# Optimization experiments

Hardware: AMD Instinct MI355X
Metric: run time of the kernel (lower is better)

The kernel has to match this reference:

```python
import jax, jax.numpy as jnp
import numpy as np


def setup_inputs() -> dict:
    key = jax.random.key(0)
    k1, k2, k3, k4 = jax.random.split(key, 4)
    N_NODES, N_RELS, N_TRIPLES, H = 100000, 100000, 300000, 256
    node_states = jax.random.normal(k1, (N_NODES, H), dtype=jnp.float32)
    rel_states = jax.random.normal(k2, (N_RELS, H), dtype=jnp.float32)
    triples = jax.random.randint(k3, (N_TRIPLES, 3), 0, N_NODES, dtype=jnp.int64)
    # nn.Linear(2H, H): weight (H, 2H) in torch; store transposed (2H, H) for x @ W
    W = jax.random.normal(k4, (2 * H, H), dtype=jnp.float32) * (1.0 / np.sqrt(2 * H))
    b = jnp.zeros((H,), dtype=jnp.float32)
    return {"node_states": node_states, "rel_states": rel_states, "triples": triples, "W": W, "b": b}


def reference(node_states, rel_states, triples, W, b):
    # triples columns: (subj_idx, rel_idx, obj_idx)
    subj_idx, rel_idx, obj_idx = triples[:, 0], triples[:, 1], triples[:, 2]
    rel = rel_states[rel_idx]                              # (T, H)
    msg_s2o = node_states[subj_idx] + rel                  # (T, H)
    msg_o2s = node_states[obj_idx] + rel                   # (T, H)
    agg = jnp.zeros_like(node_states)
    agg = agg.at[obj_idx].add(msg_s2o)
    agg = agg.at[subj_idx].add(msg_o2s)
    h = jnp.concatenate([node_states, agg], axis=-1)       # (N, 2H)
    h = h @ W + b                                          # (N, H)
    h = jax.nn.silu(h)
    return node_states + h
```

## Files before the change

kernel.cpp:

```cpp
#include <hip/hip_runtime.h>

#define H 256
typedef unsigned int  uint;
typedef unsigned short ushort;
typedef float  floatx4 __attribute__((ext_vector_type(4)));
typedef short  shortx8 __attribute__((ext_vector_type(8)));

__device__ __forceinline__ ushort bf16rn(float f) {
    uint u = __float_as_uint(f);
    u += 0x7FFF + ((u >> 16) & 1);
    return (ushort)(u >> 16);
}
__device__ __forceinline__ uint pkbf2(float a, float b) {
    return (uint)bf16rn(a) | ((uint)bf16rn(b) << 16);
}
__device__ __forceinline__ void atomic_pk_bf16(void* addr, uint v) {
    asm volatile("global_atomic_pk_add_bf16 %0, %1, off" :: "v"(addr), "v"(v) : "memory");
}
__device__ __forceinline__ void glds16(const void* g, void* l) {
    __builtin_amdgcn_global_load_lds(
        (__attribute__((address_space(1))) void*)(unsigned long long)(g),
        (__attribute__((address_space(3))) void*)(l), 16, 0, 0);
}

__global__ __launch_bounds__(256) void wt_kernel(const float* __restrict__ W,
                                                 ushort* __restrict__ Wt) {
    int k = blockIdx.x;
    int n = threadIdx.x;
    Wt[(size_t)n * 512 + k] = bf16rn(W[(size_t)k * H + n]);
}

__global__ __launch_bounds__(256) void scatter_kernel(
    const float* __restrict__ ns, const float* __restrict__ rs,
    const int* __restrict__ trip, char* __restrict__ outbase, int n_trip)
{
    int t = blockIdx.x * 2 + (threadIdx.x >> 7);
    if (t >= n_trip) return;
    int p = threadIdx.x & 127;
    int s = trip[3 * t + 0];
    int r = trip[3 * t + 1];
    int o = trip[3 * t + 2];
    float2 vs = ((const float2*)ns)[(size_t)s * 128 + p];
    float2 vo = ((const float2*)ns)[(size_t)o * 128 + p];
    float2 vr = ((const float2*)rs)[(size_t)r * 128 + p];
    uint m_s2o = pkbf2(vs.x + vr.x, vs.y + vr.y);
    uint m_o2s = pkbf2(vo.x + vr.x, vo.y + vr.y);
    atomic_pk_bf16(outbase + (size_t)o * 1024 + p * 4, m_s2o);
    atomic_pk_bf16(outbase + (size_t)s * 1024 + p * 4, m_o2s);
}

__global__ __launch_bounds__(256) void gemm_kernel(
    const float* __restrict__ ns, const float* __restrict__ aggf,
    const ushort* __restrict__ Wt, const float* __restrict__ bias,
    float* __restrict__ out, int M)
{
    __shared__ __align__(16) ushort AsP[64 * 40];
    __shared__ __align__(16) ushort AsU[64 * 32];
    __shared__ __align__(16) ushort Bs [256 * 32];

    const int tid  = threadIdx.x;
    const int wave = tid >> 6;
    const int lane = tid & 63;
    const int fm = lane & 15, fq = lane >> 4;
    const int rowBase = blockIdx.x * 64;

    floatx4 acc[4][4] = {};

    const int am = tid >> 2, akq = tid & 3;
    int arow = rowBase + am; if (arow >= M) arow = M - 1;
    const float* aptrA = ns + (size_t)arow * H + akq * 8;
    const char*  aggp  = (const char*)aggf + (size_t)arow * 1024 + akq * 16;
    const char*  wtp   = (const char*)Wt;

#pragma unroll
    for (int kt = 0; kt < 8; ++kt) {
        __syncthreads();
        float4 v0 = *(const float4*)(aptrA + kt * 32);
        float4 v1 = *(const float4*)(aptrA + kt * 32 + 4);
#pragma unroll
        for (int j = 0; j < 4; ++j)
            glds16(wtp + (size_t)(j * 64 + am) * 1024 + kt * 64 + akq * 16,
                   &Bs[j * 2048 + tid * 8]);
        uint4 pk;
        pk.x = pkbf2(v0.x, v0.y); pk.y = pkbf2(v0.z, v0.w);
        pk.z = pkbf2(v1.x, v1.y); pk.w = pkbf2(v1.z, v1.w);
        *(uint4*)&AsP[am * 40 + akq * 8] = pk;
        __syncthreads();

        shortx8 aF[4], bF[4];
#pragma unroll
        for (int mi = 0; mi < 4; ++mi)
            aF[mi] = *(const shortx8*)&AsP[(mi * 16 + fm) * 40 + fq * 8];
#pragma unroll
        for (int ni = 0; ni < 4; ++ni)
            bF[ni] = *(const shortx8*)&Bs[(wave * 64 + ni * 16 + fm) * 32 + fq * 8];
#pragma unroll
        for (int mi = 0; mi < 4; ++mi)
#pragma unroll
            for (int ni = 0; ni < 4; ++ni)
                acc[mi][ni] = __builtin_amdgcn_mfma_f32_16x16x32_bf16(
                    aF[mi], bF[ni], acc[mi][ni], 0, 0, 0);
    }

#pragma unroll
    for (int kt = 0; kt < 8; ++kt) {
        __syncthreads();
        glds16(aggp + kt * 64, &AsU[tid * 8]);
#pragma unroll
        for (int j = 0; j < 4; ++j)
            glds16(wtp + (size_t)(j * 64 + am) * 1024 + (kt + 8) * 64 + akq * 16,
                   &Bs[j * 2048 + tid * 8]);
        __syncthreads();

        shortx8 aF[4], bF[4];
#pragma unroll
        for (int mi = 0; mi < 4; ++mi)
            aF[mi] = *(const shortx8*)&AsU[(mi * 16 + fm) * 32 + fq * 8];
#pragma unroll
        for (int ni = 0; ni < 4; ++ni)
            bF[ni] = *(const shortx8*)&Bs[(wave * 64 + ni * 16 + fm) * 32 + fq * 8];
#pragma unroll
        for (int mi = 0; mi < 4; ++mi)
#pragma unroll
            for (int ni = 0; ni < 4; ++ni)
                acc[mi][ni] = __builtin_amdgcn_mfma_f32_16x16x32_bf16(
                    aF[mi], bF[ni], acc[mi][ni], 0, 0, 0);
    }

#pragma unroll
    for (int mi = 0; mi < 4; ++mi) {
#pragma unroll
        for (int ni = 0; ni < 4; ++ni) {
            int col = wave * 64 + ni * 16 + fm;
            float bc = bias[col];
#pragma unroll
            for (int r = 0; r < 4; ++r) {
                int row = rowBase + mi * 16 + fq * 4 + r;
                if (row < M) {
                    float x = acc[mi][ni][r] + bc;
                    float sg = 1.f / (1.f + __expf(-x));
                    out[(size_t)row * H + col] = ns[(size_t)row * H + col] + x * sg;
                }
            }
        }
    }
}

extern "C" void kernel_launch(void* const* d_in, const int* in_sizes, int n_in,
                              void* d_out, int out_size, void* d_ws, size_t ws_size,
                              hipStream_t stream)
{
    const float* ns   = (const float*)d_in[0];
    const float* rs   = (const float*)d_in[1];
    const int*   tp   = (const int*)d_in[2];
    const float* Wm   = (const float*)d_in[3];
    const float* bias = (const float*)d_in[4];
    const int M      = in_sizes[0] / H;
    const int n_trip = in_sizes[2] / 3;
    float*  out = (float*)d_out;
    ushort* Wt  = (ushort*)d_ws;

    hipMemsetAsync(d_out, 0, (size_t)M * H * sizeof(float), stream);
    wt_kernel<<<dim3(512), dim3(256), 0, stream>>>(Wm, Wt);
    scatter_kernel<<<dim3((n_trip + 1) / 2), dim3(256), 0, stream>>>(
        ns, rs, tp, (char*)d_out, n_trip);
    gemm_kernel<<<dim3((M + 63) / 64), dim3(256), 0, stream>>>(
        ns, out, Wt, bias, out, M);
}
```

Before: 549.0 us.

## Precast node states to bf16 in output buffer and drop LDS staging in GEMM

A prep kernel replaces the memset. It zeroes the aggregation half of each output row and writes a bf16 copy of the node states into the unused upper half. The GEMM then loads its A and B MFMA fragments straight from global memory. This removes the LDS tiles, the per-k-step barriers, and the fp32-to-bf16 packing inside the GEMM. In exchange there is an extra pass over node states before the scatter, and the GEMM now relies on L2 for fragment reuse instead of shared memory.

```diff
diff --git a/kernel.cpp b/kernel.cpp
--- a/kernel.cpp
+++ b/kernel.cpp
@@ -17,10 +17,17 @@
 __device__ __forceinline__ void atomic_pk_bf16(void* addr, uint v) {
     asm volatile("global_atomic_pk_add_bf16 %0, %1, off" :: "v"(addr), "v"(v) : "memory");
 }
-__device__ __forceinline__ void glds16(const void* g, void* l) {
-    __builtin_amdgcn_global_load_lds(
-        (__attribute__((address_space(1))) void*)(unsigned long long)(g),
-        (__attribute__((address_space(3))) void*)(l), 16, 0, 0);
+
+__global__ __launch_bounds__(256) void prep_kernel(
+    const float* __restrict__ ns, char* __restrict__ outb, int M)
+{
+    long j = (long)blockIdx.x * 256 + threadIdx.x;
+    long row = j >> 7;
+    int  p   = (int)(j & 127);
+    if (row >= M) return;
+    float2 v = ((const float2*)ns)[row * 128 + p];
+    *(uint*)(outb + row * 1024 + p * 4)       = 0u;
+    *(uint*)(outb + row * 1024 + 512 + p * 4) = pkbf2(v.x, v.y);
 }
 
 __global__ __launch_bounds__(256) void wt_kernel(const float* __restrict__ W,
@@ -50,50 +57,58 @@
 }
 
 __global__ __launch_bounds__(256) void gemm_kernel(
-    const float* __restrict__ ns, const float* __restrict__ aggf,
+    const float* __restrict__ ns, const char* __restrict__ rowbuf,
     const ushort* __restrict__ Wt, const float* __restrict__ bias,
     float* __restrict__ out, int M)
 {
-    __shared__ __align__(16) ushort AsP[64 * 40];
-    __shared__ __align__(16) ushort AsU[64 * 32];
-    __shared__ __align__(16) ushort Bs [256 * 32];
-
     const int tid  = threadIdx.x;
     const int wave = tid >> 6;
     const int lane = tid & 63;
     const int fm = lane & 15, fq = lane >> 4;
     const int rowBase = blockIdx.x * 64;
 
+    long aoff[4];
+#pragma unroll
+    for (int mi = 0; mi < 4; ++mi) {
+        int r = rowBase + mi * 16 + fm;
+        if (r >= M) r = M - 1;
+        aoff[mi] = (long)r * 1024;
+    }
+    const char* wb = (const char*)Wt;
+    const long  bn[4] = { (long)(wave * 64 +  0 + fm) * 1024,
+                          (long)(wave * 64 + 16 + fm) * 1024,
+                          (long)(wave * 64 + 32 + fm) * 1024,
+                          (long)(wave * 64 + 48 + fm) * 1024 };
+
     floatx4 acc[4][4] = {};
-
-    const int am = tid >> 2, akq = tid & 3;
-    int arow = rowBase + am; if (arow >= M) arow = M - 1;
-    const float* aptrA = ns + (size_t)arow * H + akq * 8;
-    const char*  aggp  = (const char*)aggf + (size_t)arow * 1024 + akq * 16;
-    const char*  wtp   = (const char*)Wt;
 
 #pragma unroll
     for (int kt = 0; kt < 8; ++kt) {
-        __syncthreads();
-        float4 v0 = *(const float4*)(aptrA + kt * 32);
-        float4 v1 = *(const float4*)(aptrA + kt * 32 + 4);
-#pragma unroll
-        for (int j = 0; j < 4; ++j)
-            glds16(wtp + (size_t)(j * 64 + am) * 1024 + kt * 64 + akq * 16,
-                   &Bs[j * 2048 + tid * 8]);
-        uint4 pk;
-        pk.x = pkbf2(v0.x, v0.y); pk.y = pkbf2(v0.z, v0.w);
-        pk.z = pkbf2(v1.x, v1.y); pk.w = pkbf2(v1.z, v1.w);
-        *(uint4*)&AsP[am * 40 + akq * 8] = pk;
-        __syncthreads();
-
+        const int ko = kt * 64 + fq * 16;
         shortx8 aF[4], bF[4];
 #pragma unroll
         for (int mi = 0; mi < 4; ++mi)
-            aF[mi] = *(const shortx8*)&AsP[(mi * 16 + fm) * 40 + fq * 8];
+            aF[mi] = *(const shortx8*)(rowbuf + aoff[mi] + 512 + ko);
 #pragma unroll
         for (int ni = 0; ni < 4; ++ni)
-            bF[ni] = *(const shortx8*)&Bs[(wave * 64 + ni * 16 + fm) * 32 + fq * 8];
+            bF[ni] = *(const shortx8*)(wb + bn[ni] + ko);
+#pragma unroll
+        for (int mi = 0; mi < 4; ++mi)
+#pragma unroll
+            for (int ni = 0; ni < 4; ++ni)
+                acc[mi][ni] = __builtin_amdgcn_mfma_f32_16x16x32_bf16(
+                    aF[mi], bF[ni], acc[mi][ni], 0, 0, 0);
+    }
+#pragma unroll
+    for (int kt = 0; kt < 8; ++kt) {
+        const int ko = kt * 64 + fq * 16;
+        shortx8 aF[4], bF[4];
+#pragma unroll
+        for (int mi = 0; mi < 4; ++mi)
+            aF[mi] = *(const shortx8*)(rowbuf + aoff[mi] + ko);
+#pragma unroll
+        for (int ni = 0; ni < 4; ++ni)
+            bF[ni] = *(const shortx8*)(wb + bn[ni] + 512 + ko);
 #pragma unroll
         for (int mi = 0; mi < 4; ++mi)
 #pragma unroll
@@ -102,30 +117,7 @@
                     aF[mi], bF[ni], acc[mi][ni], 0, 0, 0);
     }
 
-#pragma unroll
-    for (int kt = 0; kt < 8; ++kt) {
-        __syncthreads();
-        glds16(aggp + kt * 64, &AsU[tid * 8]);
-#pragma unroll
-        for (int j = 0; j < 4; ++j)
-            glds16(wtp + (size_t)(j * 64 + am) * 1024 + (kt + 8) * 64 + akq * 16,
-                   &Bs[j * 2048 + tid * 8]);
-        __syncthreads();
-
-        shortx8 aF[4], bF[4];
-#pragma unroll
-        for (int mi = 0; mi < 4; ++mi)
-            aF[mi] = *(const shortx8*)&AsU[(mi * 16 + fm) * 32 + fq * 8];
-#pragma unroll
-        for (int ni = 0; ni < 4; ++ni)
-            bF[ni] = *(const shortx8*)&Bs[(wave * 64 + ni * 16 + fm) * 32 + fq * 8];
-#pragma unroll
-        for (int mi = 0; mi < 4; ++mi)
-#pragma unroll
-            for (int ni = 0; ni < 4; ++ni)
-                acc[mi][ni] = __builtin_amdgcn_mfma_f32_16x16x32_bf16(
-                    aF[mi], bF[ni], acc[mi][ni], 0, 0, 0);
-    }
+    __syncthreads();
 
 #pragma unroll
     for (int mi = 0; mi < 4; ++mi) {
@@ -160,10 +152,11 @@
     float*  out = (float*)d_out;
     ushort* Wt  = (ushort*)d_ws;
 
-    hipMemsetAsync(d_out, 0, (size_t)M * H * sizeof(float), stream);
+    prep_kernel<<<dim3((M * 128 + 255) / 256), dim3(256), 0, stream>>>(
+        ns, (char*)d_out, M);
     wt_kernel<<<dim3(512), dim3(256), 0, stream>>>(Wm, Wt);
     scatter_kernel<<<dim3((n_trip + 1) / 2), dim3(256), 0, stream>>>(
         ns, rs, tp, (char*)d_out, n_trip);
     gemm_kernel<<<dim3((M + 63) / 64), dim3(256), 0, stream>>>(
-        ns, out, Wt, bias, out, M);
+        ns, (const char*)d_out, Wt, bias, out, M);
 }
```

After: 661.6 us. 1.21x slower.
